# Kernel optimization log

Hardware: AMD Instinct MI355X
Metric: run time of the kernel (lower is better)

Reference implementation:

```python
import jax, jax.numpy as jnp
import numpy as np

E, H, O = 64, 128, 16  # enc_hidden_dim, dec_hidden_dim, dec_output_dim (proj_size)
B, N, FUT = 64, 1000, 12


def _lstm_proj_cell(x, h, c, W_ih, W_hh, b_ih, b_hh, W_hr):
    # PyTorch gate order: input, forget, cell(g), output
    gates = x @ W_ih.T + h @ W_hh.T + (b_ih + b_hh)
    i, f, g, o = jnp.split(gates, 4, axis=-1)
    c_new = jax.nn.sigmoid(f) * c + jax.nn.sigmoid(i) * jnp.tanh(g)
    h_full = jax.nn.sigmoid(o) * jnp.tanh(c_new)
    h_new = h_full @ W_hr.T  # proj_size projection
    return h_new, c_new


def setup_inputs() -> dict:
    key = jax.random.key(0)
    ks = jax.random.split(key, 20)
    sc = 0.1
    inp = {
        "enc_outputs": jax.random.normal(ks[0], (B, 1, N, E), jnp.float32),
        "mean": jax.random.normal(ks[1], (B, FUT, N, O), jnp.float32),
        "s": jax.random.normal(ks[2], (1, O), jnp.float32),
        "h_0": jax.random.normal(ks[3], (2, O), jnp.float32),
        "c_0": jax.random.normal(ks[4], (2, H), jnp.float32),
        "W_ih_l0": sc * jax.random.normal(ks[5], (4 * H, E + O), jnp.float32),
        "W_hh_l0": sc * jax.random.normal(ks[6], (4 * H, O), jnp.float32),
        "b_ih_l0": sc * jax.random.normal(ks[7], (4 * H,), jnp.float32),
        "b_hh_l0": sc * jax.random.normal(ks[8], (4 * H,), jnp.float32),
        "W_hr_l0": sc * jax.random.normal(ks[9], (O, H), jnp.float32),
        "W_ih_l1": sc * jax.random.normal(ks[10], (4 * H, O), jnp.float32),
        "W_hh_l1": sc * jax.random.normal(ks[11], (4 * H, O), jnp.float32),
        "b_ih_l1": sc * jax.random.normal(ks[12], (4 * H,), jnp.float32),
        "b_hh_l1": sc * jax.random.normal(ks[13], (4 * H,), jnp.float32),
        "W_hr_l1": sc * jax.random.normal(ks[14], (O, H), jnp.float32),
        "future": FUT,
    }
    # forget-gate bias = 1.0 as in reset_bias()
    for nme in ("b_ih_l0", "b_hh_l0", "b_ih_l1", "b_hh_l1"):
        inp[nme] = inp[nme].at[H:2 * H].set(1.0)
    return inp


def _forward(enc_outputs, mean, s, h_0, c_0,
             W_ih_l0, W_hh_l0, b_ih_l0, b_hh_l0, W_hr_l0,
             W_ih_l1, W_hh_l1, b_ih_l1, b_hh_l1, W_hr_l1, future):
    b, _, n_nodes, _ = enc_outputs.shape
    enc = enc_outputs[:, 0]            # [B, N, E]
    node_mean = jnp.mean(mean, axis=1)  # [B, N, O]
    # state is carried across nodes AND timesteps: one chain of N*future steps
    node_idx = jnp.arange(n_nodes * future) // future

    last0 = jnp.broadcast_to(s[0], (b, s.shape[1]))
    h1_0 = jnp.broadcast_to(h_0[0], (b, h_0.shape[1]))
    h2_0 = jnp.broadcast_to(h_0[1], (b, h_0.shape[1]))
    c1_0 = jnp.broadcast_to(c_0[0], (b, c_0.shape[1]))
    c2_0 = jnp.broadcast_to(c_0[1], (b, c_0.shape[1]))

    def step(carry, n):
        last, h1, c1, h2, c2 = carry
        enc_t = jnp.take(enc, n, axis=1)        # [B, E]
        nm_t = jnp.take(node_mean, n, axis=1)   # [B, O]
        loop = last + nm_t                      # TFRate forced to 0.0 in source
        x = jnp.concatenate([enc_t, loop], axis=-1)
        h1, c1 = _lstm_proj_cell(x, h1, c1, W_ih_l0, W_hh_l0, b_ih_l0, b_hh_l0, W_hr_l0)
        h2, c2 = _lstm_proj_cell(h1, h2, c2, W_ih_l1, W_hh_l1, b_ih_l1, b_hh_l1, W_hr_l1)
        return (h2, h1, c1, h2, c2), h2 + nm_t

    _, outs = jax.lax.scan(step, (last0, h1_0, c1_0, h2_0, c2_0), node_idx)
    # outs: [N*future, B, O] -> [B, future, N, O]
    outs = outs.reshape(n_nodes, future, b, -1).transpose(2, 1, 0, 3)
    return outs


def reference(enc_outputs, mean, s, h_0, c_0,
              W_ih_l0, W_hh_l0, b_ih_l0, b_hh_l0, W_hr_l0,
              W_ih_l1, W_hh_l1, b_ih_l1, b_hh_l1, W_hr_l1, future):
    return _forward(enc_outputs, mean, s, h_0, c_0,
                    W_ih_l0, W_hh_l0, b_ih_l0, b_hh_l0, W_hr_l0,
                    W_ih_l1, W_hh_l1, b_ih_l1, b_hh_l1, W_hr_l1, future)
```

## Files before the change

### kernel.cpp

```cpp
#include <hip/hip_runtime.h>

#define BB 64
#define NN 1000
#define FF 12
#define EE 64
#define HH 128
#define OO 16
#define GG 512

__device__ __forceinline__ float rcp_(float x){ return __builtin_amdgcn_rcpf(x); }
__device__ __forceinline__ float sigm_(float x){ return rcp_(1.0f + __expf(-x)); }
__device__ __forceinline__ float tanh_(float x){ return 1.0f - 2.0f*rcp_(__expf(2.0f*x) + 1.0f); }

__global__ __launch_bounds__(512, 2)
void decoder_kernel(const float* __restrict__ enc,
                    const float* __restrict__ mean,
                    const float* __restrict__ sv,
                    const float* __restrict__ h0,
                    const float* __restrict__ c0,
                    const float* __restrict__ Wih0,
                    const float* __restrict__ Whh0,
                    const float* __restrict__ bih0,
                    const float* __restrict__ bhh0,
                    const float* __restrict__ Whr0,
                    const float* __restrict__ Wih1,
                    const float* __restrict__ Whh1,
                    const float* __restrict__ bih1,
                    const float* __restrict__ bhh1,
                    const float* __restrict__ Whr1,
                    float* __restrict__ out)
{
    const int t = threadIdx.x;
    const int b = blockIdx.x;

    __shared__ float s_last[OO];
    __shared__ float s_h1[OO];
    __shared__ float s_h2[OO];
    __shared__ float s_gates[GG];
    __shared__ float s_hfull[HH];
    __shared__ float s_enc[EE];
    __shared__ float s_nm[OO];

    float w_enc[EE];
    float w_loop[OO], w_hh0[OO], w_ih1[OO], w_hh1[OO];
    {
        const float* r = Wih0 + t*(EE+OO);
        #pragma unroll
        for (int e=0;e<EE;e++) w_enc[e] = r[e];
        #pragma unroll
        for (int j=0;j<OO;j++) w_loop[j] = r[EE+j];
        #pragma unroll
        for (int j=0;j<OO;j++) w_hh0[j] = Whh0[t*OO+j];
        #pragma unroll
        for (int j=0;j<OO;j++) w_ih1[j] = Wih1[t*OO+j];
        #pragma unroll
        for (int j=0;j<OO;j++) w_hh1[j] = Whh1[t*OO+j];
    }
    const float bias0 = bih0[t] + bhh0[t];
    const float bias1 = bih1[t] + bhh1[t];

    const int j16 = t >> 5;
    const int kb  = (t & 31) * 4;
    float wp0[4], wp1[4];
    #pragma unroll
    for (int u=0;u<4;u++){
        wp0[u] = Whr0[j16*HH + kb + u];
        wp1[u] = Whr1[j16*HH + kb + u];
    }

    float c1 = (t < HH) ? c0[t]      : 0.0f;
    float c2 = (t < HH) ? c0[HH + t] : 0.0f;
    if (t < OO){
        s_last[t] = sv[t];
        s_h1[t]   = h0[t];
        s_h2[t]   = h0[OO + t];
    }
    __syncthreads();

    const float* encB  = enc  + (size_t)b * NN * EE;
    const float* meanB = mean + (size_t)b * FF * NN * OO;
    float*       outB  = out  + (size_t)b * FF * NN * OO;

    const bool isTanhGate = ((t >> 7) == 2);

    for (int n = 0; n < NN; ++n){
        if (t < EE){
            s_enc[t] = encB[n*EE + t];
        } else if (t < EE + OO){
            const int j = t - EE;
            float a = 0.0f;
            #pragma unroll
            for (int f=0; f<FF; ++f) a += meanB[(f*NN + n)*OO + j];
            s_nm[j] = a * (1.0f/12.0f);
        }
        __syncthreads();

        float pre0 = bias0;
        #pragma unroll
        for (int e=0;e<EE;e++) pre0 += s_enc[e]*w_enc[e];
        #pragma unroll
        for (int j=0;j<OO;j++) pre0 += s_nm[j]*w_loop[j];

        for (int f=0; f<FF; ++f){
            float acc = pre0;
            #pragma unroll
            for (int j=0;j<OO;j++) acc += s_last[j]*w_loop[j];
            #pragma unroll
            for (int j=0;j<OO;j++) acc += s_h1[j]*w_hh0[j];
            s_gates[t] = isTanhGate ? tanh_(acc) : sigm_(acc);
            __syncthreads();

            if (t < HH){
                float iv = s_gates[t],      fv = s_gates[HH + t];
                float gv = s_gates[2*HH+t], ov = s_gates[3*HH + t];
                c1 = fv*c1 + iv*gv;
                s_hfull[t] = ov * tanh_(c1);
            }
            __syncthreads();

            {
                float p = s_hfull[kb+0]*wp0[0] + s_hfull[kb+1]*wp0[1]
                        + s_hfull[kb+2]*wp0[2] + s_hfull[kb+3]*wp0[3];
                p += __shfl_down(p, 16, 32);
                p += __shfl_down(p,  8, 32);
                p += __shfl_down(p,  4, 32);
                p += __shfl_down(p,  2, 32);
                p += __shfl_down(p,  1, 32);
                if ((t & 31) == 0) s_h1[j16] = p;
            }
            __syncthreads();

            float acc1 = bias1;
            #pragma unroll
            for (int j=0;j<OO;j++) acc1 += s_h1[j]*w_ih1[j];
            #pragma unroll
            for (int j=0;j<OO;j++) acc1 += s_h2[j]*w_hh1[j];
            s_gates[t] = isTanhGate ? tanh_(acc1) : sigm_(acc1);
            __syncthreads();

            if (t < HH){
                float iv = s_gates[t],      fv = s_gates[HH + t];
                float gv = s_gates[2*HH+t], ov = s_gates[3*HH + t];
                c2 = fv*c2 + iv*gv;
                s_hfull[t] = ov * tanh_(c2);
            }
            __syncthreads();

            {
                float p = s_hfull[kb+0]*wp1[0] + s_hfull[kb+1]*wp1[1]
                        + s_hfull[kb+2]*wp1[2] + s_hfull[kb+3]*wp1[3];
                p += __shfl_down(p, 16, 32);
                p += __shfl_down(p,  8, 32);
                p += __shfl_down(p,  4, 32);
                p += __shfl_down(p,  2, 32);
                p += __shfl_down(p,  1, 32);
                if ((t & 31) == 0){
                    s_h2[j16]   = p;
                    s_last[j16] = p;
                    outB[(f*NN + n)*OO + j16] = p + s_nm[j16];
                }
            }
            __syncthreads();
        }
    }
}

extern "C" void kernel_launch(void* const* d_in, const int* in_sizes, int n_in,
                              void* d_out, int out_size, void* d_ws, size_t ws_size,
                              hipStream_t stream) {
    const float* enc  = (const float*)d_in[0];
    const float* mean = (const float*)d_in[1];
    const float* sv   = (const float*)d_in[2];
    const float* h0   = (const float*)d_in[3];
    const float* c0   = (const float*)d_in[4];
    const float* Wih0 = (const float*)d_in[5];
    const float* Whh0 = (const float*)d_in[6];
    const float* bih0 = (const float*)d_in[7];
    const float* bhh0 = (const float*)d_in[8];
    const float* Whr0 = (const float*)d_in[9];
    const float* Wih1 = (const float*)d_in[10];
    const float* Whh1 = (const float*)d_in[11];
    const float* bih1 = (const float*)d_in[12];
    const float* bhh1 = (const float*)d_in[13];
    const float* Whr1 = (const float*)d_in[14];
    float* out = (float*)d_out;

    decoder_kernel<<<dim3(BB), dim3(512), 0, stream>>>(
        enc, mean, sv, h0, c0,
        Wih0, Whh0, bih0, bhh0, Whr0,
        Wih1, Whh1, bih1, bhh1, Whr1,
        out);
}
```

Before: 15.60 ms.

## Restructure LSTM step so each wave owns hidden units, using DPP rotations and fewer barriers

Threads are remapped so each wavefront holds all four gates for 16 hidden units. The cell update is then done with cross-lane shuffles instead of a shared-memory gate exchange, and the 16-wide matvecs rotate values through lanes with DPP row_ror. This cuts the per-timestep barriers from six to two. Projection partial sums go into small double-buffered LDS arrays, and the next node's enc/mean loads are prefetched into registers during the timestep loop. The changes add complex lane-mapping logic, a runtime DPP direction probe, and extra register pressure.

```diff
diff --git a/kernel.cpp b/kernel.cpp
--- a/kernel.cpp
+++ b/kernel.cpp
@@ -11,6 +11,12 @@
 __device__ __forceinline__ float rcp_(float x){ return __builtin_amdgcn_rcpf(x); }
 __device__ __forceinline__ float sigm_(float x){ return rcp_(1.0f + __expf(-x)); }
 __device__ __forceinline__ float tanh_(float x){ return 1.0f - 2.0f*rcp_(__expf(2.0f*x) + 1.0f); }
+
+__device__ __forceinline__ float ror1_(float x){
+    int i = __float_as_int(x);
+    i = __builtin_amdgcn_update_dpp(i, i, 0x121 , 0xF, 0xF, false);
+    return __int_as_float(i);
+}
 
 __global__ __launch_bounds__(512, 2)
 void decoder_kernel(const float* __restrict__ enc,
@@ -30,138 +36,176 @@
                     const float* __restrict__ Whr1,
                     float* __restrict__ out)
 {
-    const int t = threadIdx.x;
-    const int b = blockIdx.x;
-
-    __shared__ float s_last[OO];
-    __shared__ float s_h1[OO];
-    __shared__ float s_h2[OO];
-    __shared__ float s_gates[GG];
-    __shared__ float s_hfull[HH];
-    __shared__ float s_enc[EE];
-    __shared__ float s_nm[OO];
-
-    float w_enc[EE];
-    float w_loop[OO], w_hh0[OO], w_ih1[OO], w_hh1[OO];
-    {
-        const float* r = Wih0 + t*(EE+OO);
-        #pragma unroll
-        for (int e=0;e<EE;e++) w_enc[e] = r[e];
-        #pragma unroll
-        for (int j=0;j<OO;j++) w_loop[j] = r[EE+j];
-        #pragma unroll
-        for (int j=0;j<OO;j++) w_hh0[j] = Whh0[t*OO+j];
-        #pragma unroll
-        for (int j=0;j<OO;j++) w_ih1[j] = Wih1[t*OO+j];
-        #pragma unroll
-        for (int j=0;j<OO;j++) w_hh1[j] = Whh1[t*OO+j];
-    }
-    const float bias0 = bih0[t] + bhh0[t];
-    const float bias1 = bih1[t] + bhh1[t];
-
-    const int j16 = t >> 5;
-    const int kb  = (t & 31) * 4;
-    float wp0[4], wp1[4];
+    const int tid = threadIdx.x;
+    const int b   = blockIdx.x;
+    const int j16 = tid & 15;
+    const int tau = (tid >> 4) & 3;
+    const int wid = tid >> 6;
+    const int g   = tau*128 + wid*16 + j16;
+
+    __shared__ __align__(16) float s_pp1[2][16][12];
+    __shared__ __align__(16) float s_pp2[16][12];
+    __shared__ __align__(16) float s_enc[2][64];
+
+    int rr = __builtin_amdgcn_update_dpp(0, j16, 0x121, 0xF, 0xF, false);
+    const int dstep = (rr == ((j16 + 1) & 15)) ? 1 : 15;
+
+    float wL[16], wH[16], wI[16], wH2[16], wP0[16], wP1[16];
     #pragma unroll
-    for (int u=0;u<4;u++){
-        wp0[u] = Whr0[j16*HH + kb + u];
-        wp1[u] = Whr1[j16*HH + kb + u];
-    }
-
-    float c1 = (t < HH) ? c0[t]      : 0.0f;
-    float c2 = (t < HH) ? c0[HH + t] : 0.0f;
-    if (t < OO){
-        s_last[t] = sv[t];
-        s_h1[t]   = h0[t];
-        s_h2[t]   = h0[OO + t];
-    }
-    __syncthreads();
+    for (int q = 0; q < 16; ++q){
+        const int jj = (j16 + dstep*q) & 15;
+        wL[q]  = Wih0[g*(EE+OO) + EE + jj];
+        wH[q]  = Whh0[g*OO + jj];
+        wI[q]  = Wih1[g*OO + jj];
+        wH2[q] = Whh1[g*OO + jj];
+        wP0[q] = Whr0[j16*HH + wid*16 + jj];
+        wP1[q] = Whr1[j16*HH + wid*16 + jj];
+    }
+    const float bias0 = bih0[g] + bhh0[g];
+    const float bias1 = bih1[g] + bhh1[g];
 
     const float* encB  = enc  + (size_t)b * NN * EE;
     const float* meanB = mean + (size_t)b * FF * NN * OO;
     float*       outB  = out  + (size_t)b * FF * NN * OO;
 
-    const bool isTanhGate = ((t >> 7) == 2);
-
+    float c1 = c0[wid*16 + j16];
+    float c2 = c0[HH + wid*16 + j16];
+    const float svj = sv[j16];
+
+    if (tid < EE) s_enc[0][tid] = encB[tid];
+    float nmj;
+    {
+        float a = 0.f;
+        #pragma unroll
+        for (int ff = 0; ff < FF; ++ff) a += meanB[(ff*NN)*OO + j16];
+        nmj = a * (1.0f/12.0f);
+    }
+    if (tid < 128){
+        int j = tid >> 3, w8 = tid & 7;
+        s_pp1[0][j][w8] = (w8 == 0) ? h0[j]      : 0.f;
+        s_pp2[j][w8]    = (w8 == 0) ? h0[OO + j] : 0.f;
+    }
+    __syncthreads();
+
+    float pre0 = 0.f;
+    float nm_next = 0.f;
+    float encv = 0.f;
+    float mld[12];
+
+    int step = 0;
+    #pragma unroll 1
     for (int n = 0; n < NN; ++n){
-        if (t < EE){
-            s_enc[t] = encB[n*EE + t];
-        } else if (t < EE + OO){
-            const int j = t - EE;
-            float a = 0.0f;
-            #pragma unroll
-            for (int f=0; f<FF; ++f) a += meanB[(f*NN + n)*OO + j];
-            s_nm[j] = a * (1.0f/12.0f);
-        }
-        __syncthreads();
-
-        float pre0 = bias0;
-        #pragma unroll
-        for (int e=0;e<EE;e++) pre0 += s_enc[e]*w_enc[e];
-        #pragma unroll
-        for (int j=0;j<OO;j++) pre0 += s_nm[j]*w_loop[j];
-
-        for (int f=0; f<FF; ++f){
-            float acc = pre0;
-            #pragma unroll
-            for (int j=0;j<OO;j++) acc += s_last[j]*w_loop[j];
-            #pragma unroll
-            for (int j=0;j<OO;j++) acc += s_h1[j]*w_hh0[j];
-            s_gates[t] = isTanhGate ? tanh_(acc) : sigm_(acc);
+        #pragma unroll 1
+        for (int f = 0; f < FF; ++f, ++step){
+            const int rp = step & 1;
+            const int wq = rp ^ 1;
+
+            float4 pa = *(const float4*)&s_pp1[rp][j16][0];
+            float4 pb = *(const float4*)&s_pp1[rp][j16][4];
+            float4 qa = *(const float4*)&s_pp2[j16][0];
+            float4 qb = *(const float4*)&s_pp2[j16][4];
+            float h1j = (pa.x+pa.y)+(pa.z+pa.w)+((pb.x+pb.y)+(pb.z+pb.w));
+            float h2j = (qa.x+qa.y)+(qa.z+qa.w)+((qb.x+qb.y)+(qb.z+qb.w));
+
+            if (step > 0 && tid < OO){
+                const int fp = (f == 0) ? (FF-1) : (f-1);
+                const int np = (f == 0) ? (n-1)  : n;
+                outB[((size_t)fp*NN + np)*OO + j16] = h2j + nmj;
+            }
+            if (f == 0){
+                if (n > 0) nmj = nm_next;
+                float pre = bias0;
+                const float4* ep = (const float4*)&s_enc[n & 1][0];
+                const float4* wp = (const float4*)(Wih0 + (size_t)g*(EE+OO));
+                #pragma unroll
+                for (int e4 = 0; e4 < 16; ++e4){
+                    float4 ev = ep[e4]; float4 wv = wp[e4];
+                    pre += ev.x*wv.x + ev.y*wv.y + ev.z*wv.z + ev.w*wv.w;
+                }
+                float nv = nmj;
+                #pragma unroll
+                for (int q = 0; q < 16; ++q){ pre += nv * wL[q]; nv = ror1_(nv); }
+                pre0 = pre;
+            }
+
+            const float lastj = (step == 0) ? svj : h2j;
+
+            float aL = pre0, aH = 0.f, lv = lastj, hv = h1j;
+            #pragma unroll
+            for (int q = 0; q < 16; ++q){
+                aL += lv * wL[q];
+                aH += hv * wH[q];
+                lv = ror1_(lv); hv = ror1_(hv);
+            }
+            float gv0 = aL + aH;
+            float act = (tau == 2) ? tanh_(gv0) : sigm_(gv0);
+
+            float fc = act * c1;
+            float r1 = __shfl_xor(act, 32);
+            float P  = act * r1;
+            float s2 = (tau & 1) ? fc : P;
+            float r2 = __shfl_xor(s2, 16);
+            float cn = s2 + r2;
+            c1 = cn;
+            float hfull = r1 * tanh_(cn);
+
+            float pp = 0.f, pv = hfull;
+            #pragma unroll
+            for (int q = 0; q < 16; ++q){ pp += pv * wP0[q]; pv = ror1_(pv); }
+            if (tau == 1) s_pp1[wq][j16][wid] = pp;
             __syncthreads();
 
-            if (t < HH){
-                float iv = s_gates[t],      fv = s_gates[HH + t];
-                float gv = s_gates[2*HH+t], ov = s_gates[3*HH + t];
-                c1 = fv*c1 + iv*gv;
-                s_hfull[t] = ov * tanh_(c1);
-            }
-            __syncthreads();
-
-            {
-                float p = s_hfull[kb+0]*wp0[0] + s_hfull[kb+1]*wp0[1]
-                        + s_hfull[kb+2]*wp0[2] + s_hfull[kb+3]*wp0[3];
-                p += __shfl_down(p, 16, 32);
-                p += __shfl_down(p,  8, 32);
-                p += __shfl_down(p,  4, 32);
-                p += __shfl_down(p,  2, 32);
-                p += __shfl_down(p,  1, 32);
-                if ((t & 31) == 0) s_h1[j16] = p;
-            }
-            __syncthreads();
-
-            float acc1 = bias1;
-            #pragma unroll
-            for (int j=0;j<OO;j++) acc1 += s_h1[j]*w_ih1[j];
-            #pragma unroll
-            for (int j=0;j<OO;j++) acc1 += s_h2[j]*w_hh1[j];
-            s_gates[t] = isTanhGate ? tanh_(acc1) : sigm_(acc1);
-            __syncthreads();
-
-            if (t < HH){
-                float iv = s_gates[t],      fv = s_gates[HH + t];
-                float gv = s_gates[2*HH+t], ov = s_gates[3*HH + t];
-                c2 = fv*c2 + iv*gv;
-                s_hfull[t] = ov * tanh_(c2);
-            }
-            __syncthreads();
-
-            {
-                float p = s_hfull[kb+0]*wp1[0] + s_hfull[kb+1]*wp1[1]
-                        + s_hfull[kb+2]*wp1[2] + s_hfull[kb+3]*wp1[3];
-                p += __shfl_down(p, 16, 32);
-                p += __shfl_down(p,  8, 32);
-                p += __shfl_down(p,  4, 32);
-                p += __shfl_down(p,  2, 32);
-                p += __shfl_down(p,  1, 32);
-                if ((t & 31) == 0){
-                    s_h2[j16]   = p;
-                    s_last[j16] = p;
-                    outB[(f*NN + n)*OO + j16] = p + s_nm[j16];
-                }
-            }
+            float4 ra = *(const float4*)&s_pp1[wq][j16][0];
+            float4 rb = *(const float4*)&s_pp1[wq][j16][4];
+            float h1n = (ra.x+ra.y)+(ra.z+ra.w)+((rb.x+rb.y)+(rb.z+rb.w));
+
+            if (f == 0 && n + 1 < NN){
+                if (tid < EE) encv = encB[(size_t)(n+1)*EE + tid];
+                #pragma unroll
+                for (int ff = 0; ff < FF; ++ff)
+                    mld[ff] = meanB[((size_t)ff*NN + (n+1))*OO + j16];
+            }
+            if (f == 2 && n + 1 < NN){
+                if (tid < EE) s_enc[(n+1) & 1][tid] = encv;
+                float a = 0.f;
+                #pragma unroll
+                for (int ff = 0; ff < FF; ++ff) a += mld[ff];
+                nm_next = a * (1.0f/12.0f);
+            }
+
+            float aI = bias1, aH2 = 0.f, xv = h1n, yv = h2j;
+            #pragma unroll
+            for (int q = 0; q < 16; ++q){
+                aI  += xv * wI[q];
+                aH2 += yv * wH2[q];
+                xv = ror1_(xv); yv = ror1_(yv);
+            }
+            float gv1 = aI + aH2;
+            float act1 = (tau == 2) ? tanh_(gv1) : sigm_(gv1);
+
+            float fc1 = act1 * c2;
+            float r1b = __shfl_xor(act1, 32);
+            float Pb  = act1 * r1b;
+            float s2b = (tau & 1) ? fc1 : Pb;
+            float r2b = __shfl_xor(s2b, 16);
+            float cnb = s2b + r2b;
+            c2 = cnb;
+            float hfull2 = r1b * tanh_(cnb);
+
+            float qq = 0.f, qv = hfull2;
+            #pragma unroll
+            for (int q = 0; q < 16; ++q){ qq += qv * wP1[q]; qv = ror1_(qv); }
+            if (tau == 1) s_pp2[j16][wid] = qq;
             __syncthreads();
         }
+    }
+
+    {
+        float4 qa = *(const float4*)&s_pp2[j16][0];
+        float4 qb = *(const float4*)&s_pp2[j16][4];
+        float h2f = (qa.x+qa.y)+(qa.z+qa.w)+((qb.x+qb.y)+(qb.z+qb.w));
+        if (tid < OO)
+            outB[((size_t)(FF-1)*NN + (NN-1))*OO + j16] = h2f + nmj;
     }
 }
 
```

New measurement: 19.22 ms. 1.23x slower.

## Restructure LSTM decoder to 128 threads with per-thread gates and fewer barriers

Applied to the files above, without the earlier changes.

Each of the 128 threads now computes all four gates for its hidden unit, so the gate exchange through shared memory and several barriers per step are removed. The output projection is split across two waves with DPP reductions, and the partial sums are double-buffered so only two barriers remain per timestep. Encoder and mean rows for the next node are prefetched a few steps early, and encoder weights are re-read from global memory once per node rather than held in registers. In exchange, the block uses fewer threads, each holding many more register weights, and the intra-wave LDS handoff relies on a waitcnt instead of a barrier.

```diff
diff --git a/kernel.cpp b/kernel.cpp
--- a/kernel.cpp
+++ b/kernel.cpp
@@ -6,13 +6,18 @@
 #define EE 64
 #define HH 128
 #define OO 16
-#define GG 512
 
 __device__ __forceinline__ float rcp_(float x){ return __builtin_amdgcn_rcpf(x); }
 __device__ __forceinline__ float sigm_(float x){ return rcp_(1.0f + __expf(-x)); }
 __device__ __forceinline__ float tanh_(float x){ return 1.0f - 2.0f*rcp_(__expf(2.0f*x) + 1.0f); }
 
-__global__ __launch_bounds__(512, 2)
+template<int CTRL>
+__device__ __forceinline__ float dppadd_(float v){
+    int s = __builtin_amdgcn_update_dpp(0, __float_as_int(v), CTRL, 0xF, 0xF, true);
+    return v + __int_as_float(s);
+}
+
+__global__ __launch_bounds__(128, 1)
 void decoder_kernel(const float* __restrict__ enc,
                     const float* __restrict__ mean,
                     const float* __restrict__ sv,
@@ -30,138 +35,235 @@
                     const float* __restrict__ Whr1,
                     float* __restrict__ out)
 {
-    const int t = threadIdx.x;
-    const int b = blockIdx.x;
-
-    __shared__ float s_last[OO];
-    __shared__ float s_h1[OO];
-    __shared__ float s_h2[OO];
-    __shared__ float s_gates[GG];
-    __shared__ float s_hfull[HH];
-    __shared__ float s_enc[EE];
-    __shared__ float s_nm[OO];
-
-    float w_enc[EE];
-    float w_loop[OO], w_hh0[OO], w_ih1[OO], w_hh1[OO];
-    {
-        const float* r = Wih0 + t*(EE+OO);
+    const int t  = threadIdx.x;
+    const int b  = blockIdx.x;
+    const int k  = t;
+    const int w  = t >> 6;
+    const int l  = t & 63;
+    const int pj = l >> 2;
+    const int pc4= l & 3;
+
+    __shared__ __align__(16) float s_pp1[2][2][16];
+    __shared__ __align__(16) float s_pp2[2][2][16];
+    __shared__ __align__(16) float s_hf[128];
+    __shared__ __align__(16) float s_encN[64];
+    __shared__ __align__(16) float s_nm[16];
+    __shared__ __align__(16) float s_nmN[16];
+    __shared__ __align__(16) float s_sv[16];
+
+    float wl0[64], wh0[64], wi1[64], wh1[64];
+    float bias1r[4], pre0r[4];
+    #pragma unroll
+    for (int tau=0; tau<4; ++tau){
+        const int g = tau*128 + k;
+        const float4* pL = (const float4*)(Wih0 + (size_t)g*(EE+OO) + EE);
+        const float4* pH = (const float4*)(Whh0 + (size_t)g*OO);
+        const float4* pI = (const float4*)(Wih1 + (size_t)g*OO);
+        const float4* pG = (const float4*)(Whh1 + (size_t)g*OO);
         #pragma unroll
-        for (int e=0;e<EE;e++) w_enc[e] = r[e];
-        #pragma unroll
-        for (int j=0;j<OO;j++) w_loop[j] = r[EE+j];
-        #pragma unroll
-        for (int j=0;j<OO;j++) w_hh0[j] = Whh0[t*OO+j];
-        #pragma unroll
-        for (int j=0;j<OO;j++) w_ih1[j] = Wih1[t*OO+j];
-        #pragma unroll
-        for (int j=0;j<OO;j++) w_hh1[j] = Whh1[t*OO+j];
-    }
-    const float bias0 = bih0[t] + bhh0[t];
-    const float bias1 = bih1[t] + bhh1[t];
-
-    const int j16 = t >> 5;
-    const int kb  = (t & 31) * 4;
-    float wp0[4], wp1[4];
+        for (int i=0;i<4;i++){
+            float4 v;
+            v = pL[i]; wl0[tau*16+4*i+0]=v.x; wl0[tau*16+4*i+1]=v.y; wl0[tau*16+4*i+2]=v.z; wl0[tau*16+4*i+3]=v.w;
+            v = pH[i]; wh0[tau*16+4*i+0]=v.x; wh0[tau*16+4*i+1]=v.y; wh0[tau*16+4*i+2]=v.z; wh0[tau*16+4*i+3]=v.w;
+            v = pI[i]; wi1[tau*16+4*i+0]=v.x; wi1[tau*16+4*i+1]=v.y; wi1[tau*16+4*i+2]=v.z; wi1[tau*16+4*i+3]=v.w;
+            v = pG[i]; wh1[tau*16+4*i+0]=v.x; wh1[tau*16+4*i+1]=v.y; wh1[tau*16+4*i+2]=v.z; wh1[tau*16+4*i+3]=v.w;
+        }
+        bias1r[tau] = bih1[g] + bhh1[g];
+        pre0r[tau]  = 0.f;
+    }
+    float wq0[16], wq1[16];
     #pragma unroll
-    for (int u=0;u<4;u++){
-        wp0[u] = Whr0[j16*HH + kb + u];
-        wp1[u] = Whr1[j16*HH + kb + u];
-    }
-
-    float c1 = (t < HH) ? c0[t]      : 0.0f;
-    float c2 = (t < HH) ? c0[HH + t] : 0.0f;
-    if (t < OO){
-        s_last[t] = sv[t];
-        s_h1[t]   = h0[t];
-        s_h2[t]   = h0[OO + t];
-    }
-    __syncthreads();
+    for (int i=0;i<4;i++){
+        float4 v0 = *(const float4*)(Whr0 + (size_t)pj*HH + w*64 + pc4*16 + 4*i);
+        float4 v1 = *(const float4*)(Whr1 + (size_t)pj*HH + w*64 + pc4*16 + 4*i);
+        wq0[4*i+0]=v0.x; wq0[4*i+1]=v0.y; wq0[4*i+2]=v0.z; wq0[4*i+3]=v0.w;
+        wq1[4*i+0]=v1.x; wq1[4*i+1]=v1.y; wq1[4*i+2]=v1.z; wq1[4*i+3]=v1.w;
+    }
+
+    float c1v = c0[k];
+    float c2v = c0[HH + k];
 
     const float* encB  = enc  + (size_t)b * NN * EE;
     const float* meanB = mean + (size_t)b * FF * NN * OO;
     float*       outB  = out  + (size_t)b * FF * NN * OO;
 
-    const bool isTanhGate = ((t >> 7) == 2);
-
+    if (t < 16){
+        s_pp1[0][0][t] = h0[t];      s_pp1[0][1][t] = 0.f;
+        s_pp2[0][0][t] = h0[OO + t]; s_pp2[0][1][t] = 0.f;
+        s_sv[t] = sv[t];
+        ((float4*)s_encN)[t] = ((const float4*)encB)[t];
+    } else if (t < 32){
+        const int j = t - 16;
+        float a = 0.f;
+        #pragma unroll
+        for (int ff=0; ff<FF; ++ff) a += meanB[((size_t)ff*NN)*OO + j];
+        float v = a * (1.0f/12.0f);
+        s_nm[j] = v; s_nmN[j] = v;
+    }
+    __syncthreads();
+
+    float4 ef = make_float4(0.f,0.f,0.f,0.f);
+    float  nmr[12];
+    #pragma unroll
+    for (int i=0;i<12;i++) nmr[i]=0.f;
+
+    int step = 0;
+    #pragma unroll 1
     for (int n = 0; n < NN; ++n){
-        if (t < EE){
-            s_enc[t] = encB[n*EE + t];
-        } else if (t < EE + OO){
-            const int j = t - EE;
-            float a = 0.0f;
+        #pragma unroll 1
+        for (int f = 0; f < FF; ++f, ++step){
+            const int rp = step & 1;
+
+            float h1v[16], h2v[16], lv[16];
+            {
+                const float4* pa = (const float4*)&s_pp1[rp][0][0];
+                const float4* pb = (const float4*)&s_pp1[rp][1][0];
+                const float4* qa = (const float4*)&s_pp2[rp][0][0];
+                const float4* qb = (const float4*)&s_pp2[rp][1][0];
+                #pragma unroll
+                for (int i=0;i<4;i++){
+                    float4 a = pa[i], c = pb[i];
+                    h1v[4*i+0]=a.x+c.x; h1v[4*i+1]=a.y+c.y; h1v[4*i+2]=a.z+c.z; h1v[4*i+3]=a.w+c.w;
+                    float4 d = qa[i], e = qb[i];
+                    h2v[4*i+0]=d.x+e.x; h2v[4*i+1]=d.y+e.y; h2v[4*i+2]=d.z+e.z; h2v[4*i+3]=d.w+e.w;
+                }
+                const float* nms = (f==0) ? s_nmN : s_nm;
+                const float4* nm4 = (const float4*)nms;
+                #pragma unroll
+                for (int i=0;i<4;i++){
+                    float4 m = nm4[i];
+                    lv[4*i+0]=h2v[4*i+0]+m.x; lv[4*i+1]=h2v[4*i+1]+m.y;
+                    lv[4*i+2]=h2v[4*i+2]+m.z; lv[4*i+3]=h2v[4*i+3]+m.w;
+                }
+                if (step == 0){
+                    const float4* sv4 = (const float4*)s_sv;
+                    #pragma unroll
+                    for (int i=0;i<4;i++){
+                        float4 s0 = sv4[i]; float4 m = nm4[i];
+                        lv[4*i+0]=s0.x+m.x; lv[4*i+1]=s0.y+m.y; lv[4*i+2]=s0.z+m.z; lv[4*i+3]=s0.w+m.w;
+                    }
+                }
+            }
+
+            if (step > 0 && t < OO){
+                const int fp = (f==0) ? (FF-1) : (f-1);
+                const int np = (f==0) ? (n-1)  : n;
+                float val = s_pp2[rp][0][t] + s_pp2[rp][1][t] + s_nm[t];
+                outB[((size_t)fp*NN + np)*OO + t] = val;
+            }
+
+            if (f == 0){
+                if (t < OO) s_nm[t] = s_nmN[t];
+                const float4* ep = (const float4*)s_encN;
+                #pragma unroll
+                for (int tau=0; tau<4; ++tau){
+                    const int g = tau*128 + k;
+                    const float4* wp = (const float4*)(Wih0 + (size_t)g*(EE+OO));
+                    float s = bih0[g] + bhh0[g];
+                    #pragma unroll
+                    for (int e=0;e<16;e++){
+                        float4 wv = wp[e], evv = ep[e];
+                        s += evv.x*wv.x + evv.y*wv.y + evv.z*wv.z + evv.w*wv.w;
+                    }
+                    pre0r[tau] = s;
+                }
+            }
+
+            float a0=pre0r[0], a1=pre0r[1], a2=pre0r[2], a3=pre0r[3];
             #pragma unroll
-            for (int f=0; f<FF; ++f) a += meanB[(f*NN + n)*OO + j];
-            s_nm[j] = a * (1.0f/12.0f);
-        }
-        __syncthreads();
-
-        float pre0 = bias0;
-        #pragma unroll
-        for (int e=0;e<EE;e++) pre0 += s_enc[e]*w_enc[e];
-        #pragma unroll
-        for (int j=0;j<OO;j++) pre0 += s_nm[j]*w_loop[j];
-
-        for (int f=0; f<FF; ++f){
-            float acc = pre0;
+            for (int j=0;j<16;j++){
+                float xl = lv[j], xh = h1v[j];
+                a0 += xl*wl0[j];     a0 += xh*wh0[j];
+                a1 += xl*wl0[16+j]; a1 += xh*wh0[16+j];
+                a2 += xl*wl0[32+j]; a2 += xh*wh0[32+j];
+                a3 += xl*wl0[48+j]; a3 += xh*wh0[48+j];
+            }
+            {
+                float iv=sigm_(a0), fv=sigm_(a1), gv=tanh_(a2), ov=sigm_(a3);
+                c1v = fv*c1v + iv*gv;
+                float hf = ov * tanh_(c1v);
+                s_hf[((k>>4)<<2) + (((k>>2)&3)<<5) + (k&3)] = hf;
+            }
+            asm volatile("s_waitcnt lgkmcnt(0)" ::: "memory");
+            {
+                float pr = 0.f;
+                #pragma unroll
+                for (int i=0;i<4;i++){
+                    float4 h4 = *(const float4*)&s_hf[(4*w + pc4)*4 + 32*i];
+                    pr += h4.x*wq0[4*i+0] + h4.y*wq0[4*i+1] + h4.z*wq0[4*i+2] + h4.w*wq0[4*i+3];
+                }
+                pr = dppadd_<0x111>(pr);
+                pr = dppadd_<0x112>(pr);
+                if (pc4 == 3) s_pp1[rp^1][w][pj] = pr;
+            }
+            __syncthreads();
+
+            float h1n[16];
+            {
+                const float4* na = (const float4*)&s_pp1[rp^1][0][0];
+                const float4* nb = (const float4*)&s_pp1[rp^1][1][0];
+                #pragma unroll
+                for (int i=0;i<4;i++){
+                    float4 a = na[i], c = nb[i];
+                    h1n[4*i+0]=a.x+c.x; h1n[4*i+1]=a.y+c.y; h1n[4*i+2]=a.z+c.z; h1n[4*i+3]=a.w+c.w;
+                }
+            }
+
+            if (f == 8 && n+1 < NN){
+                if (t < 16){
+                    ef = ((const float4*)(encB + (size_t)(n+1)*EE))[t];
+                } else if (t < 32){
+                    const int j = t - 16;
+                    #pragma unroll
+                    for (int ff=0; ff<FF; ++ff)
+                        nmr[ff] = meanB[((size_t)ff*NN + (n+1))*OO + j];
+                }
+            }
+            if (f == 10 && n+1 < NN){
+                if (t < 16){
+                    ((float4*)s_encN)[t] = ef;
+                } else if (t < 32){
+                    float a = 0.f;
+                    #pragma unroll
+                    for (int ff=0; ff<FF; ++ff) a += nmr[ff];
+                    s_nmN[t-16] = a * (1.0f/12.0f);
+                }
+            }
+
+            float b0=bias1r[0], b1=bias1r[1], b2=bias1r[2], b3=bias1r[3];
             #pragma unroll
-            for (int j=0;j<OO;j++) acc += s_last[j]*w_loop[j];
-            #pragma unroll
-            for (int j=0;j<OO;j++) acc += s_h1[j]*w_hh0[j];
-            s_gates[t] = isTanhGate ? tanh_(acc) : sigm_(acc);
-            __syncthreads();
-
-            if (t < HH){
-                float iv = s_gates[t],      fv = s_gates[HH + t];
-                float gv = s_gates[2*HH+t], ov = s_gates[3*HH + t];
-                c1 = fv*c1 + iv*gv;
-                s_hfull[t] = ov * tanh_(c1);
-            }
-            __syncthreads();
-
-            {
-                float p = s_hfull[kb+0]*wp0[0] + s_hfull[kb+1]*wp0[1]
-                        + s_hfull[kb+2]*wp0[2] + s_hfull[kb+3]*wp0[3];
-                p += __shfl_down(p, 16, 32);
-                p += __shfl_down(p,  8, 32);
-                p += __shfl_down(p,  4, 32);
-                p += __shfl_down(p,  2, 32);
-                p += __shfl_down(p,  1, 32);
-                if ((t & 31) == 0) s_h1[j16] = p;
-            }
-            __syncthreads();
-
-            float acc1 = bias1;
-            #pragma unroll
-            for (int j=0;j<OO;j++) acc1 += s_h1[j]*w_ih1[j];
-            #pragma unroll
-            for (int j=0;j<OO;j++) acc1 += s_h2[j]*w_hh1[j];
-            s_gates[t] = isTanhGate ? tanh_(acc1) : sigm_(acc1);
-            __syncthreads();
-
-            if (t < HH){
-                float iv = s_gates[t],      fv = s_gates[HH + t];
-                float gv = s_gates[2*HH+t], ov = s_gates[3*HH + t];
-                c2 = fv*c2 + iv*gv;
-                s_hfull[t] = ov * tanh_(c2);
-            }
-            __syncthreads();
-
-            {
-                float p = s_hfull[kb+0]*wp1[0] + s_hfull[kb+1]*wp1[1]
-                        + s_hfull[kb+2]*wp1[2] + s_hfull[kb+3]*wp1[3];
-                p += __shfl_down(p, 16, 32);
-                p += __shfl_down(p,  8, 32);
-                p += __shfl_down(p,  4, 32);
-                p += __shfl_down(p,  2, 32);
-                p += __shfl_down(p,  1, 32);
-                if ((t & 31) == 0){
-                    s_h2[j16]   = p;
-                    s_last[j16] = p;
-                    outB[(f*NN + n)*OO + j16] = p + s_nm[j16];
-                }
+            for (int j=0;j<16;j++){
+                float x1 = h1n[j], x2 = h2v[j];
+                b0 += x1*wi1[j];     b0 += x2*wh1[j];
+                b1 += x1*wi1[16+j]; b1 += x2*wh1[16+j];
+                b2 += x1*wi1[32+j]; b2 += x2*wh1[32+j];
+                b3 += x1*wi1[48+j]; b3 += x2*wh1[48+j];
+            }
+            {
+                float iv=sigm_(b0), fv=sigm_(b1), gv=tanh_(b2), ov=sigm_(b3);
+                c2v = fv*c2v + iv*gv;
+                float hf = ov * tanh_(c2v);
+                s_hf[((k>>4)<<2) + (((k>>2)&3)<<5) + (k&3)] = hf;
+            }
+            asm volatile("s_waitcnt lgkmcnt(0)" ::: "memory");
+            {
+                float pr = 0.f;
+                #pragma unroll
+                for (int i=0;i<4;i++){
+                    float4 h4 = *(const float4*)&s_hf[(4*w + pc4)*4 + 32*i];
+                    pr += h4.x*wq1[4*i+0] + h4.y*wq1[4*i+1] + h4.z*wq1[4*i+2] + h4.w*wq1[4*i+3];
+                }
+                pr = dppadd_<0x111>(pr);
+                pr = dppadd_<0x112>(pr);
+                if (pc4 == 3) s_pp2[rp^1][w][pj] = pr;
             }
             __syncthreads();
         }
+    }
+
+    if (t < OO){
+        float val = s_pp2[0][0][t] + s_pp2[0][1][t] + s_nm[t];
+        outB[((size_t)(FF-1)*NN + (NN-1))*OO + t] = val;
     }
 }
 
@@ -185,7 +287,7 @@
     const float* Whr1 = (const float*)d_in[14];
     float* out = (float*)d_out;
 
-    decoder_kernel<<<dim3(BB), dim3(512), 0, stream>>>(
+    decoder_kernel<<<dim3(BB), dim3(128), 0, stream>>>(
         enc, mean, sv, h0, c0,
         Wih0, Whh0, bih0, bhh0, Whr0,
         Wih1, Whh1, bih1, bhh1, Whr1,
```

After: 34.81 ms. +123.1%, slower.

## Restructure LSTM step to cut barriers via gate-interleaved lanes and DPP exchange

Applied to the files above, without the earlier changes.

Gates are remapped so the four gates of each hidden unit sit in adjacent lanes, which lets the cell update run on DPP quad swizzles instead of a shared-memory gate array plus a barrier. The projection uses ds_bpermute with an LDS atomicAdd into double-buffered h arrays, bringing the per-step barrier count from six to two. Since last equals h2, that term is folded into the W_loop dot product, with a one-time correction on the first step. The next node's enc and mean are prefetched a few steps early. In exchange the indexing is considerably more intricate, and LDS float atomics make the summation order nondeterministic.

```diff
diff --git a/kernel.cpp b/kernel.cpp
--- a/kernel.cpp
+++ b/kernel.cpp
@@ -6,11 +6,23 @@
 #define EE 64
 #define HH 128
 #define OO 16
-#define GG 512
 
 __device__ __forceinline__ float rcp_(float x){ return __builtin_amdgcn_rcpf(x); }
-__device__ __forceinline__ float sigm_(float x){ return rcp_(1.0f + __expf(-x)); }
 __device__ __forceinline__ float tanh_(float x){ return 1.0f - 2.0f*rcp_(__expf(2.0f*x) + 1.0f); }
+
+template<int CTRL>
+__device__ __forceinline__ float qswz_(float x){
+    int r = __builtin_amdgcn_update_dpp(0, __float_as_int(x), CTRL, 0xF, 0xF, true);
+    return __int_as_float(r);
+}
+__device__ __forceinline__ float bperm_(int byteIdx, float v){
+    return __int_as_float(__builtin_amdgcn_ds_bpermute(byteIdx, __float_as_int(v)));
+}
+__device__ __forceinline__ void barrier_lds_(){
+    asm volatile("s_waitcnt lgkmcnt(0)" ::: "memory");
+    __builtin_amdgcn_s_barrier();
+    asm volatile("" ::: "memory");
+}
 
 __global__ __launch_bounds__(512, 2)
 void decoder_kernel(const float* __restrict__ enc,
@@ -30,139 +42,212 @@
                     const float* __restrict__ Whr1,
                     float* __restrict__ out)
 {
-    const int t = threadIdx.x;
-    const int b = blockIdx.x;
-
-    __shared__ float s_last[OO];
-    __shared__ float s_h1[OO];
-    __shared__ float s_h2[OO];
-    __shared__ float s_gates[GG];
-    __shared__ float s_hfull[HH];
-    __shared__ float s_enc[EE];
-    __shared__ float s_nm[OO];
-
-    float w_enc[EE];
-    float w_loop[OO], w_hh0[OO], w_ih1[OO], w_hh1[OO];
+    const int t   = threadIdx.x;
+    const int b   = blockIdx.x;
+    const int l   = t & 63;
+    const int w   = t >> 6;
+    const int k   = t >> 2;
+    const int tau = t & 3;
+    const int g   = tau*HH + k;
+    const int pj  = l >> 2;
+    const int pc  = l & 3;
+
+    __shared__ __align__(16) float s_h1a[2][OO];
+    __shared__ __align__(16) float s_h2a[2][OO];
+    __shared__ __align__(16) float s_nm[2][OO];
+    __shared__ __align__(16) float s_enc[EE];
+
+    float wl0[16], wh0[16], wi1[16], wh1[16], wq0[4], wq1[4];
     {
-        const float* r = Wih0 + t*(EE+OO);
+        const float4* pL = (const float4*)(Wih0 + (size_t)g*(EE+OO) + EE);
+        const float4* pH = (const float4*)(Whh0 + (size_t)g*OO);
+        const float4* pI = (const float4*)(Wih1 + (size_t)g*OO);
+        const float4* pG = (const float4*)(Whh1 + (size_t)g*OO);
         #pragma unroll
-        for (int e=0;e<EE;e++) w_enc[e] = r[e];
-        #pragma unroll
-        for (int j=0;j<OO;j++) w_loop[j] = r[EE+j];
-        #pragma unroll
-        for (int j=0;j<OO;j++) w_hh0[j] = Whh0[t*OO+j];
-        #pragma unroll
-        for (int j=0;j<OO;j++) w_ih1[j] = Wih1[t*OO+j];
-        #pragma unroll
-        for (int j=0;j<OO;j++) w_hh1[j] = Whh1[t*OO+j];
-    }
-    const float bias0 = bih0[t] + bhh0[t];
-    const float bias1 = bih1[t] + bhh1[t];
-
-    const int j16 = t >> 5;
-    const int kb  = (t & 31) * 4;
-    float wp0[4], wp1[4];
+        for (int i=0;i<4;i++){
+            float4 v;
+            v=pL[i]; wl0[4*i]=v.x; wl0[4*i+1]=v.y; wl0[4*i+2]=v.z; wl0[4*i+3]=v.w;
+            v=pH[i]; wh0[4*i]=v.x; wh0[4*i+1]=v.y; wh0[4*i+2]=v.z; wh0[4*i+3]=v.w;
+            v=pI[i]; wi1[4*i]=v.x; wi1[4*i+1]=v.y; wi1[4*i+2]=v.z; wi1[4*i+3]=v.w;
+            v=pG[i]; wh1[4*i]=v.x; wh1[4*i+1]=v.y; wh1[4*i+2]=v.z; wh1[4*i+3]=v.w;
+        }
+        float4 q0 = *(const float4*)(Whr0 + (size_t)pj*HH + w*16 + pc*4);
+        float4 q1 = *(const float4*)(Whr1 + (size_t)pj*HH + w*16 + pc*4);
+        wq0[0]=q0.x; wq0[1]=q0.y; wq0[2]=q0.z; wq0[3]=q0.w;
+        wq1[0]=q1.x; wq1[1]=q1.y; wq1[2]=q1.z; wq1[3]=q1.w;
+    }
+    const float bias0r = bih0[g] + bhh0[g];
+    const float bias1r = bih1[g] + bhh1[g];
+    float corr1 = 0.f;
     #pragma unroll
-    for (int u=0;u<4;u++){
-        wp0[u] = Whr0[j16*HH + kb + u];
-        wp1[u] = Whr1[j16*HH + kb + u];
-    }
-
-    float c1 = (t < HH) ? c0[t]      : 0.0f;
-    float c2 = (t < HH) ? c0[HH + t] : 0.0f;
-    if (t < OO){
-        s_last[t] = sv[t];
-        s_h1[t]   = h0[t];
-        s_h2[t]   = h0[OO + t];
-    }
-    __syncthreads();
+    for (int i=0;i<4;i++){
+        float4 hv  = *(const float4*)(h0 + OO + 4*i);
+        float4 svv = *(const float4*)(sv + 4*i);
+        corr1 += (hv.x-svv.x)*wh1[4*i]   + (hv.y-svv.y)*wh1[4*i+1]
+               + (hv.z-svv.z)*wh1[4*i+2] + (hv.w-svv.w)*wh1[4*i+3];
+    }
+    const float am = (tau==2) ? 2.0f : 1.0f;
+
+    float c1v = c0[k];
+    float c2v = c0[HH+k];
 
     const float* encB  = enc  + (size_t)b * NN * EE;
     const float* meanB = mean + (size_t)b * FF * NN * OO;
     float*       outB  = out  + (size_t)b * FF * NN * OO;
 
-    const bool isTanhGate = ((t >> 7) == 2);
-
+    if (t < OO){
+        s_h1a[0][t] = h0[t];
+        s_h1a[1][t] = 0.f;
+        s_h2a[0][t] = sv[t];
+        s_h2a[1][t] = 0.f;
+        ((float4*)s_enc)[t] = ((const float4*)encB)[t];
+    } else if (t < 2*OO){
+        const int j = t - OO;
+        float a = 0.f;
+        #pragma unroll
+        for (int ff=0; ff<FF; ++ff) a += meanB[((size_t)ff*NN)*OO + j];
+        s_nm[0][j] = a * (1.0f/12.0f);
+    }
+    __syncthreads();
+
+    float4 ef = make_float4(0.f,0.f,0.f,0.f);
+    float nmr[12];
+    #pragma unroll
+    for (int i=0;i<12;i++) nmr[i]=0.f;
+    float pre0 = 0.f;
+
+    int step = 0;
+    #pragma unroll 1
     for (int n = 0; n < NN; ++n){
-        if (t < EE){
-            s_enc[t] = encB[n*EE + t];
-        } else if (t < EE + OO){
-            const int j = t - EE;
-            float a = 0.0f;
+        #pragma unroll 1
+        for (int f = 0; f < FF; ++f, ++step){
+            const int rp = step & 1;
+
+            float h1v[16], h2v[16];
+            {
+                const float4* pa = (const float4*)s_h1a[rp];
+                const float4* pb = (const float4*)s_h2a[rp];
+                #pragma unroll
+                for (int i=0;i<4;i++){
+                    float4 a = pa[i]; h1v[4*i]=a.x; h1v[4*i+1]=a.y; h1v[4*i+2]=a.z; h1v[4*i+3]=a.w;
+                    float4 c = pb[i]; h2v[4*i]=c.x; h2v[4*i+1]=c.y; h2v[4*i+2]=c.z; h2v[4*i+3]=c.w;
+                }
+            }
+            if (step > 0 && t < OO){
+                const int fp = (f==0) ? (FF-1) : (f-1);
+                const int np = (f==0) ? (n-1)  : n;
+                const int sl = (f==0) ? ((n&1)^1) : (n&1);
+                outB[((size_t)fp*NN + np)*OO + t] = s_h2a[rp][t] + s_nm[sl][t];
+            }
+            if (t < OO) s_h2a[rp^1][t] = 0.f;
+
+            if (f == 0){
+                float s = bias0r;
+                const float4* wp = (const float4*)(Wih0 + (size_t)g*(EE+OO));
+                const float4* ep = (const float4*)s_enc;
+                #pragma unroll
+                for (int e=0;e<16;e++){
+                    float4 wv = wp[e], evv = ep[e];
+                    s += evv.x*wv.x + evv.y*wv.y + evv.z*wv.z + evv.w*wv.w;
+                }
+                const float4* nm4 = (const float4*)s_nm[n&1];
+                #pragma unroll
+                for (int i=0;i<4;i++){
+                    float4 m = nm4[i];
+                    s += m.x*wl0[4*i] + m.y*wl0[4*i+1] + m.z*wl0[4*i+2] + m.w*wl0[4*i+3];
+                }
+                pre0 = s;
+            }
+
+            float aL=0.f, aH=0.f;
             #pragma unroll
-            for (int f=0; f<FF; ++f) a += meanB[(f*NN + n)*OO + j];
-            s_nm[j] = a * (1.0f/12.0f);
+            for (int j=0;j<16;j++){ aL += h2v[j]*wl0[j]; aH += h1v[j]*wh0[j]; }
+            float x0  = pre0 + aL + aH;
+            float act = 1.f - am * rcp_(__expf(am*x0) + 1.f);
+
+            float r2 = qswz_<0x4E>(act);
+            float P  = act * r2;
+            float s2 = (tau==1) ? act*c1v : P;
+            float cn = s2 + qswz_<0xB1>(s2);
+            c1v = cn;
+            float tc = tanh_(cn);
+            float hf = act * qswz_<0x4E>(tc);
+
+            {
+                const int bb = pc*64 + 12;
+                float v0 = bperm_(bb,    hf);
+                float v1 = bperm_(bb+16, hf);
+                float v2 = bperm_(bb+32, hf);
+                float v3 = bperm_(bb+48, hf);
+                float pr = v0*wq0[0] + v1*wq0[1] + v2*wq0[2] + v3*wq0[3];
+                pr += qswz_<0xB1>(pr);
+                pr += qswz_<0x4E>(pr);
+                if (pc == 0) atomicAdd(&s_h1a[rp^1][pj], pr);
+            }
+            barrier_lds_();
+
+            float h1n[16];
+            {
+                const float4* na = (const float4*)s_h1a[rp^1];
+                #pragma unroll
+                for (int i=0;i<4;i++){
+                    float4 a = na[i]; h1n[4*i]=a.x; h1n[4*i+1]=a.y; h1n[4*i+2]=a.z; h1n[4*i+3]=a.w;
+                }
+            }
+            if (t < OO) s_h1a[rp][t] = 0.f;
+
+            if (f == 8 && n+1 < NN){
+                if (t < OO){
+                    ef = ((const float4*)(encB + (size_t)(n+1)*EE))[t];
+                } else if (t < 2*OO){
+                    const int j = t - OO;
+                    #pragma unroll
+                    for (int ff=0; ff<FF; ++ff) nmr[ff] = meanB[((size_t)ff*NN + (n+1))*OO + j];
+                }
+            }
+            if (f == 10 && n+1 < NN){
+                if (t < OO){
+                    ((float4*)s_enc)[t] = ef;
+                } else if (t < 2*OO){
+                    float a = 0.f;
+                    #pragma unroll
+                    for (int ff=0; ff<FF; ++ff) a += nmr[ff];
+                    s_nm[(n+1)&1][t-OO] = a * (1.0f/12.0f);
+                }
+            }
+
+            float aI=0.f, aH2=0.f;
+            #pragma unroll
+            for (int j=0;j<16;j++){ aI += h1n[j]*wi1[j]; aH2 += h2v[j]*wh1[j]; }
+            float x1 = bias1r + aI + aH2;
+            if (step == 0) x1 += corr1;
+            float act1 = 1.f - am * rcp_(__expf(am*x1) + 1.f);
+
+            float r2b = qswz_<0x4E>(act1);
+            float Pb  = act1 * r2b;
+            float s2b = (tau==1) ? act1*c2v : Pb;
+            float cnb = s2b + qswz_<0xB1>(s2b);
+            c2v = cnb;
+            float tcb = tanh_(cnb);
+            float hf2 = act1 * qswz_<0x4E>(tcb);
+
+            {
+                const int bb = pc*64 + 12;
+                float v0 = bperm_(bb,    hf2);
+                float v1 = bperm_(bb+16, hf2);
+                float v2 = bperm_(bb+32, hf2);
+                float v3 = bperm_(bb+48, hf2);
+                float pr = v0*wq1[0] + v1*wq1[1] + v2*wq1[2] + v3*wq1[3];
+                pr += qswz_<0xB1>(pr);
+                pr += qswz_<0x4E>(pr);
+                if (pc == 0) atomicAdd(&s_h2a[rp^1][pj], pr);
+            }
+            barrier_lds_();
         }
-        __syncthreads();
-
-        float pre0 = bias0;
-        #pragma unroll
-        for (int e=0;e<EE;e++) pre0 += s_enc[e]*w_enc[e];
-        #pragma unroll
-        for (int j=0;j<OO;j++) pre0 += s_nm[j]*w_loop[j];
-
-        for (int f=0; f<FF; ++f){
-            float acc = pre0;
-            #pragma unroll
-            for (int j=0;j<OO;j++) acc += s_last[j]*w_loop[j];
-            #pragma unroll
-            for (int j=0;j<OO;j++) acc += s_h1[j]*w_hh0[j];
-            s_gates[t] = isTanhGate ? tanh_(acc) : sigm_(acc);
-            __syncthreads();
-
-            if (t < HH){
-                float iv = s_gates[t],      fv = s_gates[HH + t];
-                float gv = s_gates[2*HH+t], ov = s_gates[3*HH + t];
-                c1 = fv*c1 + iv*gv;
-                s_hfull[t] = ov * tanh_(c1);
-            }
-            __syncthreads();
-
-            {
-                float p = s_hfull[kb+0]*wp0[0] + s_hfull[kb+1]*wp0[1]
-                        + s_hfull[kb+2]*wp0[2] + s_hfull[kb+3]*wp0[3];
-                p += __shfl_down(p, 16, 32);
-                p += __shfl_down(p,  8, 32);
-                p += __shfl_down(p,  4, 32);
-                p += __shfl_down(p,  2, 32);
-                p += __shfl_down(p,  1, 32);
-                if ((t & 31) == 0) s_h1[j16] = p;
-            }
-            __syncthreads();
-
-            float acc1 = bias1;
-            #pragma unroll
-            for (int j=0;j<OO;j++) acc1 += s_h1[j]*w_ih1[j];
-            #pragma unroll
-            for (int j=0;j<OO;j++) acc1 += s_h2[j]*w_hh1[j];
-            s_gates[t] = isTanhGate ? tanh_(acc1) : sigm_(acc1);
-            __syncthreads();
-
-            if (t < HH){
-                float iv = s_gates[t],      fv = s_gates[HH + t];
-                float gv = s_gates[2*HH+t], ov = s_gates[3*HH + t];
-                c2 = fv*c2 + iv*gv;
-                s_hfull[t] = ov * tanh_(c2);
-            }
-            __syncthreads();
-
-            {
-                float p = s_hfull[kb+0]*wp1[0] + s_hfull[kb+1]*wp1[1]
-                        + s_hfull[kb+2]*wp1[2] + s_hfull[kb+3]*wp1[3];
-                p += __shfl_down(p, 16, 32);
-                p += __shfl_down(p,  8, 32);
-                p += __shfl_down(p,  4, 32);
-                p += __shfl_down(p,  2, 32);
-                p += __shfl_down(p,  1, 32);
-                if ((t & 31) == 0){
-                    s_h2[j16]   = p;
-                    s_last[j16] = p;
-                    outB[(f*NN + n)*OO + j16] = p + s_nm[j16];
-                }
-            }
-            __syncthreads();
-        }
-    }
+    }
+
+    if (t < OO)
+        outB[((size_t)(FF-1)*NN + (NN-1))*OO + t] = s_h2a[0][t] + s_nm[(NN-1)&1][t];
 }
 
 extern "C" void kernel_launch(void* const* d_in, const int* in_sizes, int n_in,
```

Measured after the change: 16.17 ms. 3.6% more time.
